# Kernel optimization log

Hardware: AMD Instinct MI355X
Metric: run time of the kernel (lower is better)

The kernel has to match this reference:

```python
import jax, jax.numpy as jnp
import numpy as np

HID = 512
ROLES = 64

def setup_inputs() -> dict:
    key = jax.random.key(0)
    k1, k2, k3, k4, k5 = jax.random.split(key, 5)
    pred_input = jax.random.normal(k1, (8, 512, HID), dtype=jnp.float32)
    args_input = jax.random.normal(k2, (8, 512, HID), dtype=jnp.float32)
    # learned params (orthogonal init approximated by scaled normal for testing)
    U = jax.random.normal(k3, (HID, ROLES, HID), dtype=jnp.float32) * 0.02
    bias1 = jax.random.normal(k4, (1, HID * ROLES), dtype=jnp.float32) * 0.02
    bias2 = jax.random.normal(k5, (1, ROLES), dtype=jnp.float32) * 0.02
    return {"pred_input": pred_input, "args_input": args_input,
            "U": U, "bias1": bias1, "bias2": bias2}

def reference(pred_input, args_input, U, bias1, bias2):
    # dropout p=0.0 -> identity (eval behavior)
    b, t, h = pred_input.shape
    n = b * t
    pred = pred_input.reshape(n, h)          # [n, h]
    args = args_input.reshape(n, h)          # [n, h]
    # first = pred @ U.view(h, R*h) + bias1  -> [n, R*h]
    first = pred @ U.reshape(h, -1) + bias1
    # batched bilinear reduction: [n, R, h] x [n, h] -> [n, R]
    out = jnp.einsum('nrk,nk->nr', first.reshape(n, ROLES, h), args)
    return out + bias2
```

## Files before the change

### kernel.cpp

```cpp
#include <hip/hip_runtime.h>
#include <stdint.h>


#define HID   512
#define ROLES 64
#define NTOK  4096
#define BM    256
#define BN    256
#define BK    64

typedef __attribute__((ext_vector_type(8))) _Float16 f16x8;
typedef __attribute__((ext_vector_type(4))) _Float16 f16x4;
typedef __attribute__((ext_vector_type(4))) float    f32x4;

__device__ __forceinline__ void async16(const void* g, void* l) {
  __builtin_amdgcn_global_load_lds(
      (const __attribute__((address_space(1))) uint32_t*)g,
      (__attribute__((address_space(3))) uint32_t*)l, 16, 0, 0);
}

__global__ __launch_bounds__(256) void prep_fused(
    const float* __restrict__ pred_in, _Float16* __restrict__ predf,
    const float* __restrict__ U, _Float16* __restrict__ ut) {
  __shared__ float tile[128][65];
  const int bx = blockIdx.x;
  const int t  = threadIdx.x;

  if (bx >= 2048) {
    const int idx = (bx - 2048) * 256 + t;
    const float4 v = ((const float4*)pred_in)[idx];
    f16x4 o;
    o[0] = (_Float16)v.x; o[1] = (_Float16)v.y;
    o[2] = (_Float16)v.z; o[3] = (_Float16)v.w;
    ((f16x4*)predf)[idx] = o;
    return;
  }

  const int kb = bx & 7, hb = (bx >> 3) & 3, r = bx >> 5;
  const int h0 = hb * 128, k0 = kb * 64;
  const int rr = t >> 4, c4 = (t & 15) * 4;
#pragma unroll
  for (int pass = 0; pass < 8; pass++) {
    const int row = pass * 16 + rr;
    const float4 v = *(const float4*)(U + ((size_t)(h0 + row) * ROLES + r) * HID + k0 + c4);
    tile[row][c4 + 0] = v.x; tile[row][c4 + 1] = v.y;
    tile[row][c4 + 2] = v.z; tile[row][c4 + 3] = v.w;
  }
  __syncthreads();
  const int kr = t >> 4, hc = (t & 15) * 8;
#pragma unroll
  for (int pass = 0; pass < 4; pass++) {
    const int k = pass * 16 + kr;
    alignas(16) _Float16 hbuf[8];
#pragma unroll
    for (int j = 0; j < 8; j++) hbuf[j] = (_Float16)tile[hc + j][k];
    *(uint4*)(ut + ((size_t)r * HID + k0 + k) * HID + h0 + hc) = *(const uint4*)hbuf;
  }
}

__global__ __launch_bounds__(512, 2) void bilinear_mfma(
    const _Float16* __restrict__ predf, const _Float16* __restrict__ utf,
    const float* __restrict__ args, const float* __restrict__ bias1,
    float* __restrict__ part) {
  __shared__ _Float16 lds[2][32768];

  const int nblk = blockIdx.x, mblk = blockIdx.y, r = blockIdx.z;
  const int m0 = mblk * BM, n0 = nblk * BN;
  const int tid  = threadIdx.x;
  const int lane = tid & 63, wid = tid >> 6;
  const int col  = lane & 15, quad = lane >> 4;
  const int wr = wid >> 2, wc = wid & 3;
  const int wm = wr * 128, wn = wc * 64;

  const int i_loc = tid >> 3;
  const int ko    = ((tid & 7) ^ (i_loc & 7)) * 8;
  const size_t offA = (size_t)(m0 + i_loc) * HID + ko;
  const size_t offB = ((size_t)r * HID + n0 + i_loc) * HID + ko;
  const int ldsOff = tid * 8;

  const int slotL8 = (quad ^ (col & 7)) * 8;
  const int slotH8 = slotL8 ^ 32;
  int rowA[8], rowB[4];
#pragma unroll
  for (int mt = 0; mt < 8; mt++) rowA[mt] = (wm + mt * 16 + col) * BK;
#pragma unroll
  for (int nt = 0; nt < 4; nt++) rowB[nt] = (wn + nt * 16 + col) * BK;

  f32x4 acc[8][4];
#pragma unroll
  for (int a = 0; a < 8; a++)
#pragma unroll
    for (int b = 0; b < 4; b++) acc[a][b] = (f32x4){0.f, 0.f, 0.f, 0.f};

  auto STAGE = [&](int t, int buf) {
    _Float16* bA = &lds[buf][0];
    _Float16* bB = &lds[buf][16384];
    const size_t kof = (size_t)t * BK;
#pragma unroll
    for (int c = 0; c < 4; c++) {
      async16(predf + offA + (size_t)(c * 64) * HID + kof, bA + c * 4096 + ldsOff);
      async16(utf   + offB + (size_t)(c * 64) * HID + kof, bB + c * 4096 + ldsOff);
    }
  };

  STAGE(0, 0);
  STAGE(1, 1);
  asm volatile("s_waitcnt vmcnt(8)" ::: "memory");
  __builtin_amdgcn_s_barrier();
  __builtin_amdgcn_sched_barrier(0);

  for (int t = 0; t < 8; ++t) {
    const _Float16* bA = &lds[t & 1][0];
    const _Float16* bB = &lds[t & 1][16384];

    f16x8 aL[4], aH[4], bL[2], bH[2], cL[2], cH[2];

#pragma unroll
    for (int mt = 0; mt < 4; mt++) {
      aL[mt] = *(const f16x8*)(bA + rowA[mt] + slotL8);
      aH[mt] = *(const f16x8*)(bA + rowA[mt] + slotH8);
    }
#pragma unroll
    for (int nt = 0; nt < 2; nt++) {
      bL[nt] = *(const f16x8*)(bB + rowB[nt] + slotL8);
      bH[nt] = *(const f16x8*)(bB + rowB[nt] + slotH8);
    }
    __builtin_amdgcn_s_setprio(1);
#pragma unroll
    for (int mt = 0; mt < 4; mt++)
#pragma unroll
      for (int nt = 0; nt < 2; nt++) {
        acc[mt][nt] = __builtin_amdgcn_mfma_f32_16x16x32_f16(aL[mt], bL[nt], acc[mt][nt], 0, 0, 0);
        acc[mt][nt] = __builtin_amdgcn_mfma_f32_16x16x32_f16(aH[mt], bH[nt], acc[mt][nt], 0, 0, 0);
      }
    __builtin_amdgcn_s_setprio(0);
    __builtin_amdgcn_s_barrier();
    __builtin_amdgcn_sched_barrier(0);

#pragma unroll
    for (int nt = 0; nt < 2; nt++) {
      cL[nt] = *(const f16x8*)(bB + rowB[nt + 2] + slotL8);
      cH[nt] = *(const f16x8*)(bB + rowB[nt + 2] + slotH8);
    }
    __builtin_amdgcn_s_setprio(1);
#pragma unroll
    for (int mt = 0; mt < 4; mt++)
#pragma unroll
      for (int nt = 0; nt < 2; nt++) {
        acc[mt][nt + 2] = __builtin_amdgcn_mfma_f32_16x16x32_f16(aL[mt], cL[nt], acc[mt][nt + 2], 0, 0, 0);
        acc[mt][nt + 2] = __builtin_amdgcn_mfma_f32_16x16x32_f16(aH[mt], cH[nt], acc[mt][nt + 2], 0, 0, 0);
      }
    __builtin_amdgcn_s_setprio(0);
    __builtin_amdgcn_s_barrier();
    __builtin_amdgcn_sched_barrier(0);

#pragma unroll
    for (int mt = 0; mt < 4; mt++) {
      aL[mt] = *(const f16x8*)(bA + rowA[mt + 4] + slotL8);
      aH[mt] = *(const f16x8*)(bA + rowA[mt + 4] + slotH8);
    }
    __builtin_amdgcn_s_setprio(1);
#pragma unroll
    for (int mt = 0; mt < 4; mt++)
#pragma unroll
      for (int nt = 0; nt < 2; nt++) {
        acc[mt + 4][nt + 2] = __builtin_amdgcn_mfma_f32_16x16x32_f16(aL[mt], cL[nt], acc[mt + 4][nt + 2], 0, 0, 0);
        acc[mt + 4][nt + 2] = __builtin_amdgcn_mfma_f32_16x16x32_f16(aH[mt], cH[nt], acc[mt + 4][nt + 2], 0, 0, 0);
      }
    __builtin_amdgcn_s_setprio(0);
    __builtin_amdgcn_s_barrier();
    __builtin_amdgcn_sched_barrier(0);

#pragma unroll
    for (int nt = 0; nt < 2; nt++) {
      bL[nt] = *(const f16x8*)(bB + rowB[nt] + slotL8);
      bH[nt] = *(const f16x8*)(bB + rowB[nt] + slotH8);
    }
    __builtin_amdgcn_s_setprio(1);
#pragma unroll
    for (int mt = 0; mt < 4; mt++)
#pragma unroll
      for (int nt = 0; nt < 2; nt++) {
        acc[mt + 4][nt] = __builtin_amdgcn_mfma_f32_16x16x32_f16(aL[mt], bL[nt], acc[mt + 4][nt], 0, 0, 0);
        acc[mt + 4][nt] = __builtin_amdgcn_mfma_f32_16x16x32_f16(aH[mt], bH[nt], acc[mt + 4][nt], 0, 0, 0);
      }
    __builtin_amdgcn_s_setprio(0);
    __builtin_amdgcn_s_barrier();
    __builtin_amdgcn_sched_barrier(0);

    if (t < 6) {
      STAGE(t + 2, t & 1);
      asm volatile("s_waitcnt vmcnt(8)" ::: "memory");
    } else if (t == 6) {
      asm volatile("s_waitcnt vmcnt(0)" ::: "memory");
    }
    __builtin_amdgcn_s_barrier();
    __builtin_amdgcn_sched_barrier(0);
  }

  float b1v[4];
#pragma unroll
  for (int nt = 0; nt < 4; nt++)
    b1v[nt] = bias1[r * HID + n0 + wn + nt * 16 + col];

  float sval[8][4];
#pragma unroll
  for (int mt = 0; mt < 8; mt++) {
#pragma unroll
    for (int reg = 0; reg < 4; reg++) {
      const int m = m0 + wm + mt * 16 + quad * 4 + reg;
      const float* arow = args + (size_t)m * HID + n0 + wn + col;
      float s = 0.f;
#pragma unroll
      for (int nt = 0; nt < 4; nt++)
        s += (acc[mt][nt][reg] + b1v[nt]) * arow[nt * 16];
      s += __shfl_xor(s, 1);
      s += __shfl_xor(s, 2);
      s += __shfl_xor(s, 4);
      s += __shfl_xor(s, 8);
      sval[mt][reg] = s;
    }
  }

  float* red = (float*)&lds[0][0];
  if (wc != 0 && col == 0) {
#pragma unroll
    for (int mt = 0; mt < 8; mt++)
#pragma unroll
      for (int reg = 0; reg < 4; reg++)
        red[(wc - 1) * 256 + wm + mt * 16 + quad * 4 + reg] = sval[mt][reg];
  }
  __syncthreads();
  if (wc == 0 && col == 0) {
    float* pbase = part + (((size_t)nblk * ROLES + r) << 12) + m0;
#pragma unroll
    for (int mt = 0; mt < 8; mt++) {
      const int row = wm + mt * 16 + quad * 4;
      float4 v;
      v.x = sval[mt][0] + red[row + 0] + red[256 + row + 0] + red[512 + row + 0];
      v.y = sval[mt][1] + red[row + 1] + red[256 + row + 1] + red[512 + row + 1];
      v.z = sval[mt][2] + red[row + 2] + red[256 + row + 2] + red[512 + row + 2];
      v.w = sval[mt][3] + red[row + 3] + red[256 + row + 3] + red[512 + row + 3];
      *(float4*)(pbase + row) = v;
    }
  }
}

__global__ __launch_bounds__(256) void reduce_k(const float* __restrict__ part,
                                                const float* __restrict__ b2,
                                                float* __restrict__ out) {
  const int idx = blockIdx.x * 256 + threadIdx.x;
  const int m = idx >> 6, r = idx & (ROLES - 1);
  float v = b2[r];
#pragma unroll
  for (int nb = 0; nb < 2; nb++)
    v += part[(((size_t)nb * ROLES + r) << 12) + m];
  out[idx] = v;
}

__global__ __launch_bounds__(256) void fallback_k(
    const float* __restrict__ pred, const float* __restrict__ args,
    const float* __restrict__ U, const float* __restrict__ b1,
    const float* __restrict__ b2, float* __restrict__ out) {
  const int idx = blockIdx.x * 256 + threadIdx.x;
  const int r = idx >> 12;
  const int n = idx & (NTOK - 1);
  const float* arow = args + (size_t)n * HID;
  const float* prow = pred + (size_t)n * HID;
  float acc = 0.f;
  for (int h = 0; h < HID; h++) {
    const float* urow = U + ((size_t)h * ROLES + r) * HID;
    float s = 0.f;
    for (int k = 0; k < HID; k++) s = fmaf(urow[k], arow[k], s);
    acc = fmaf(prow[h], s, acc);
  }
  float sb = 0.f;
  const float* brow = b1 + (size_t)r * HID;
  for (int k = 0; k < HID; k++) sb = fmaf(brow[k], arow[k], sb);
  out[(size_t)n * ROLES + r] = acc + sb + b2[r];
}

extern "C" void kernel_launch(void* const* d_in, const int* in_sizes, int n_in,
                              void* d_out, int out_size, void* d_ws, size_t ws_size,
                              hipStream_t stream) {
  const float* pred = (const float*)d_in[0];
  const float* args = (const float*)d_in[1];
  const float* U    = (const float*)d_in[2];
  const float* b1   = (const float*)d_in[3];
  const float* b2   = (const float*)d_in[4];
  float* out = (float*)d_out;

  const size_t PRED_ELEMS = (size_t)NTOK * HID;
  const size_t U_ELEMS    = (size_t)HID * ROLES * HID;
  const size_t PART_ELEMS = (size_t)2 * ROLES * NTOK;
  const size_t WS_NEEDED  = (PRED_ELEMS + U_ELEMS) * sizeof(_Float16)
                          + PART_ELEMS * sizeof(float);

  if (ws_size < WS_NEEDED) {
    hipLaunchKernelGGL(fallback_k, dim3((NTOK * ROLES) / 256), dim3(256), 0, stream,
                       pred, args, U, b1, b2, out);
    return;
  }

  _Float16* predf = (_Float16*)d_ws;
  _Float16* utf   = predf + PRED_ELEMS;
  float*    partb = (float*)(utf + U_ELEMS);

  hipLaunchKernelGGL(prep_fused, dim3(4096), dim3(256), 0, stream,
                     pred, predf, U, utf);
  hipLaunchKernelGGL(bilinear_mfma, dim3(HID / BN, NTOK / BM, ROLES), dim3(512), 0, stream,
                     predf, utf, args, b1, partb);
  hipLaunchKernelGGL(reduce_k, dim3((NTOK * ROLES) / 256), dim3(256), 0, stream,
                     partb, b2, out);
}
```

Before: 267.1 us.

## Loop both N halves inside each block and fold bias2 in, dropping reduce kernel

Each block now loops over both 256-wide N halves of the hidden dimension and keeps a running per-row bilinear sum. Bias2 is added in the epilogue, which writes the output directly, so the partial buffer and the separate reduce kernel go away. This saves one launch and a round trip to global memory. In exchange the grid is halved (1024 blocks), so parallelism and latency hiding drop, and the output writes are strided by ROLES and scattered rather than issued as float4 stores.

```diff
diff --git a/kernel.cpp b/kernel.cpp
--- a/kernel.cpp
+++ b/kernel.cpp
@@ -61,11 +61,11 @@
 __global__ __launch_bounds__(512, 2) void bilinear_mfma(
     const _Float16* __restrict__ predf, const _Float16* __restrict__ utf,
     const float* __restrict__ args, const float* __restrict__ bias1,
-    float* __restrict__ part) {
+    const float* __restrict__ bias2, float* __restrict__ out) {
   __shared__ _Float16 lds[2][32768];
 
-  const int nblk = blockIdx.x, mblk = blockIdx.y, r = blockIdx.z;
-  const int m0 = mblk * BM, n0 = nblk * BN;
+  const int mblk = blockIdx.x, r = blockIdx.y;
+  const int m0 = mblk * BM;
   const int tid  = threadIdx.x;
   const int lane = tid & 63, wid = tid >> 6;
   const int col  = lane & 15, quad = lane >> 4;
@@ -74,8 +74,8 @@
 
   const int i_loc = tid >> 3;
   const int ko    = ((tid & 7) ^ (i_loc & 7)) * 8;
-  const size_t offA = (size_t)(m0 + i_loc) * HID + ko;
-  const size_t offB = ((size_t)r * HID + n0 + i_loc) * HID + ko;
+  const size_t offA  = (size_t)(m0 + i_loc) * HID + ko;
+  const size_t offB0 = ((size_t)r * HID + i_loc) * HID + ko;
   const int ldsOff = tid * 8;
 
   const int slotL8 = (quad ^ (col & 7)) * 8;
@@ -86,139 +86,149 @@
 #pragma unroll
   for (int nt = 0; nt < 4; nt++) rowB[nt] = (wn + nt * 16 + col) * BK;
 
-  f32x4 acc[8][4];
+  float sval[8][4];
 #pragma unroll
   for (int a = 0; a < 8; a++)
 #pragma unroll
-    for (int b = 0; b < 4; b++) acc[a][b] = (f32x4){0.f, 0.f, 0.f, 0.f};
-
-  auto STAGE = [&](int t, int buf) {
-    _Float16* bA = &lds[buf][0];
-    _Float16* bB = &lds[buf][16384];
-    const size_t kof = (size_t)t * BK;
-#pragma unroll
-    for (int c = 0; c < 4; c++) {
-      async16(predf + offA + (size_t)(c * 64) * HID + kof, bA + c * 4096 + ldsOff);
-      async16(utf   + offB + (size_t)(c * 64) * HID + kof, bB + c * 4096 + ldsOff);
-    }
-  };
-
-  STAGE(0, 0);
-  STAGE(1, 1);
-  asm volatile("s_waitcnt vmcnt(8)" ::: "memory");
-  __builtin_amdgcn_s_barrier();
-  __builtin_amdgcn_sched_barrier(0);
-
-  for (int t = 0; t < 8; ++t) {
-    const _Float16* bA = &lds[t & 1][0];
-    const _Float16* bB = &lds[t & 1][16384];
-
-    f16x8 aL[4], aH[4], bL[2], bH[2], cL[2], cH[2];
-
-#pragma unroll
-    for (int mt = 0; mt < 4; mt++) {
-      aL[mt] = *(const f16x8*)(bA + rowA[mt] + slotL8);
-      aH[mt] = *(const f16x8*)(bA + rowA[mt] + slotH8);
-    }
-#pragma unroll
-    for (int nt = 0; nt < 2; nt++) {
-      bL[nt] = *(const f16x8*)(bB + rowB[nt] + slotL8);
-      bH[nt] = *(const f16x8*)(bB + rowB[nt] + slotH8);
-    }
-    __builtin_amdgcn_s_setprio(1);
-#pragma unroll
-    for (int mt = 0; mt < 4; mt++)
-#pragma unroll
-      for (int nt = 0; nt < 2; nt++) {
-        acc[mt][nt] = __builtin_amdgcn_mfma_f32_16x16x32_f16(aL[mt], bL[nt], acc[mt][nt], 0, 0, 0);
-        acc[mt][nt] = __builtin_amdgcn_mfma_f32_16x16x32_f16(aH[mt], bH[nt], acc[mt][nt], 0, 0, 0);
-      }
-    __builtin_amdgcn_s_setprio(0);
+    for (int b = 0; b < 4; b++) sval[a][b] = 0.f;
+
+  for (int half = 0; half < 2; ++half) {
+    const int n0 = half * BN;
+    const size_t offB = offB0 + (size_t)n0 * HID;
+
+    f32x4 acc[8][4];
+#pragma unroll
+    for (int a = 0; a < 8; a++)
+#pragma unroll
+      for (int b = 0; b < 4; b++) acc[a][b] = (f32x4){0.f, 0.f, 0.f, 0.f};
+
+    auto STAGE = [&](int t, int buf) {
+      _Float16* bA = &lds[buf][0];
+      _Float16* bB = &lds[buf][16384];
+      const size_t kof = (size_t)t * BK;
+#pragma unroll
+      for (int c = 0; c < 4; c++) {
+        async16(predf + offA + (size_t)(c * 64) * HID + kof, bA + c * 4096 + ldsOff);
+        async16(utf   + offB + (size_t)(c * 64) * HID + kof, bB + c * 4096 + ldsOff);
+      }
+    };
+
+    STAGE(0, 0);
+    STAGE(1, 1);
+    asm volatile("s_waitcnt vmcnt(8)" ::: "memory");
     __builtin_amdgcn_s_barrier();
     __builtin_amdgcn_sched_barrier(0);
 
-#pragma unroll
-    for (int nt = 0; nt < 2; nt++) {
-      cL[nt] = *(const f16x8*)(bB + rowB[nt + 2] + slotL8);
-      cH[nt] = *(const f16x8*)(bB + rowB[nt + 2] + slotH8);
+    for (int t = 0; t < 8; ++t) {
+      const _Float16* bA = &lds[t & 1][0];
+      const _Float16* bB = &lds[t & 1][16384];
+
+      f16x8 aL[4], aH[4], bL[2], bH[2], cL[2], cH[2];
+
+#pragma unroll
+      for (int mt = 0; mt < 4; mt++) {
+        aL[mt] = *(const f16x8*)(bA + rowA[mt] + slotL8);
+        aH[mt] = *(const f16x8*)(bA + rowA[mt] + slotH8);
+      }
+#pragma unroll
+      for (int nt = 0; nt < 2; nt++) {
+        bL[nt] = *(const f16x8*)(bB + rowB[nt] + slotL8);
+        bH[nt] = *(const f16x8*)(bB + rowB[nt] + slotH8);
+      }
+      __builtin_amdgcn_s_setprio(1);
+#pragma unroll
+      for (int mt = 0; mt < 4; mt++)
+#pragma unroll
+        for (int nt = 0; nt < 2; nt++) {
+          acc[mt][nt] = __builtin_amdgcn_mfma_f32_16x16x32_f16(aL[mt], bL[nt], acc[mt][nt], 0, 0, 0);
+          acc[mt][nt] = __builtin_amdgcn_mfma_f32_16x16x32_f16(aH[mt], bH[nt], acc[mt][nt], 0, 0, 0);
+        }
+      __builtin_amdgcn_s_setprio(0);
+      __builtin_amdgcn_s_barrier();
+      __builtin_amdgcn_sched_barrier(0);
+
+#pragma unroll
+      for (int nt = 0; nt < 2; nt++) {
+        cL[nt] = *(const f16x8*)(bB + rowB[nt + 2] + slotL8);
+        cH[nt] = *(const f16x8*)(bB + rowB[nt + 2] + slotH8);
+      }
+      __builtin_amdgcn_s_setprio(1);
+#pragma unroll
+      for (int mt = 0; mt < 4; mt++)
+#pragma unroll
+        for (int nt = 0; nt < 2; nt++) {
+          acc[mt][nt + 2] = __builtin_amdgcn_mfma_f32_16x16x32_f16(aL[mt], cL[nt], acc[mt][nt + 2], 0, 0, 0);
+          acc[mt][nt + 2] = __builtin_amdgcn_mfma_f32_16x16x32_f16(aH[mt], cH[nt], acc[mt][nt + 2], 0, 0, 0);
+        }
+      __builtin_amdgcn_s_setprio(0);
+      __builtin_amdgcn_s_barrier();
+      __builtin_amdgcn_sched_barrier(0);
+
+#pragma unroll
+      for (int mt = 0; mt < 4; mt++) {
+        aL[mt] = *(const f16x8*)(bA + rowA[mt + 4] + slotL8);
+        aH[mt] = *(const f16x8*)(bA + rowA[mt + 4] + slotH8);
+      }
+      __builtin_amdgcn_s_setprio(1);
+#pragma unroll
+      for (int mt = 0; mt < 4; mt++)
+#pragma unroll
+        for (int nt = 0; nt < 2; nt++) {
+          acc[mt + 4][nt + 2] = __builtin_amdgcn_mfma_f32_16x16x32_f16(aL[mt], cL[nt], acc[mt + 4][nt + 2], 0, 0, 0);
+          acc[mt + 4][nt + 2] = __builtin_amdgcn_mfma_f32_16x16x32_f16(aH[mt], cH[nt], acc[mt + 4][nt + 2], 0, 0, 0);
+        }
+      __builtin_amdgcn_s_setprio(0);
+      __builtin_amdgcn_s_barrier();
+      __builtin_amdgcn_sched_barrier(0);
+
+#pragma unroll
+      for (int nt = 0; nt < 2; nt++) {
+        bL[nt] = *(const f16x8*)(bB + rowB[nt] + slotL8);
+        bH[nt] = *(const f16x8*)(bB + rowB[nt] + slotH8);
+      }
+      __builtin_amdgcn_s_setprio(1);
+#pragma unroll
+      for (int mt = 0; mt < 4; mt++)
+#pragma unroll
+        for (int nt = 0; nt < 2; nt++) {
+          acc[mt + 4][nt] = __builtin_amdgcn_mfma_f32_16x16x32_f16(aL[mt], bL[nt], acc[mt + 4][nt], 0, 0, 0);
+          acc[mt + 4][nt] = __builtin_amdgcn_mfma_f32_16x16x32_f16(aH[mt], bH[nt], acc[mt + 4][nt], 0, 0, 0);
+        }
+      __builtin_amdgcn_s_setprio(0);
+      __builtin_amdgcn_s_barrier();
+      __builtin_amdgcn_sched_barrier(0);
+
+      if (t < 6) {
+        STAGE(t + 2, t & 1);
+        asm volatile("s_waitcnt vmcnt(8)" ::: "memory");
+      } else if (t == 6) {
+        asm volatile("s_waitcnt vmcnt(0)" ::: "memory");
+      }
+      __builtin_amdgcn_s_barrier();
+      __builtin_amdgcn_sched_barrier(0);
     }
-    __builtin_amdgcn_s_setprio(1);
-#pragma unroll
-    for (int mt = 0; mt < 4; mt++)
-#pragma unroll
-      for (int nt = 0; nt < 2; nt++) {
-        acc[mt][nt + 2] = __builtin_amdgcn_mfma_f32_16x16x32_f16(aL[mt], cL[nt], acc[mt][nt + 2], 0, 0, 0);
-        acc[mt][nt + 2] = __builtin_amdgcn_mfma_f32_16x16x32_f16(aH[mt], cH[nt], acc[mt][nt + 2], 0, 0, 0);
-      }
-    __builtin_amdgcn_s_setprio(0);
-    __builtin_amdgcn_s_barrier();
-    __builtin_amdgcn_sched_barrier(0);
-
-#pragma unroll
-    for (int mt = 0; mt < 4; mt++) {
-      aL[mt] = *(const f16x8*)(bA + rowA[mt + 4] + slotL8);
-      aH[mt] = *(const f16x8*)(bA + rowA[mt + 4] + slotH8);
-    }
-    __builtin_amdgcn_s_setprio(1);
-#pragma unroll
-    for (int mt = 0; mt < 4; mt++)
-#pragma unroll
-      for (int nt = 0; nt < 2; nt++) {
-        acc[mt + 4][nt + 2] = __builtin_amdgcn_mfma_f32_16x16x32_f16(aL[mt], cL[nt], acc[mt + 4][nt + 2], 0, 0, 0);
-        acc[mt + 4][nt + 2] = __builtin_amdgcn_mfma_f32_16x16x32_f16(aH[mt], cH[nt], acc[mt + 4][nt + 2], 0, 0, 0);
-      }
-    __builtin_amdgcn_s_setprio(0);
-    __builtin_amdgcn_s_barrier();
-    __builtin_amdgcn_sched_barrier(0);
-
-#pragma unroll
-    for (int nt = 0; nt < 2; nt++) {
-      bL[nt] = *(const f16x8*)(bB + rowB[nt] + slotL8);
-      bH[nt] = *(const f16x8*)(bB + rowB[nt] + slotH8);
-    }
-    __builtin_amdgcn_s_setprio(1);
-#pragma unroll
-    for (int mt = 0; mt < 4; mt++)
-#pragma unroll
-      for (int nt = 0; nt < 2; nt++) {
-        acc[mt + 4][nt] = __builtin_amdgcn_mfma_f32_16x16x32_f16(aL[mt], bL[nt], acc[mt + 4][nt], 0, 0, 0);
-        acc[mt + 4][nt] = __builtin_amdgcn_mfma_f32_16x16x32_f16(aH[mt], bH[nt], acc[mt + 4][nt], 0, 0, 0);
-      }
-    __builtin_amdgcn_s_setprio(0);
-    __builtin_amdgcn_s_barrier();
-    __builtin_amdgcn_sched_barrier(0);
-
-    if (t < 6) {
-      STAGE(t + 2, t & 1);
-      asm volatile("s_waitcnt vmcnt(8)" ::: "memory");
-    } else if (t == 6) {
-      asm volatile("s_waitcnt vmcnt(0)" ::: "memory");
-    }
-    __builtin_amdgcn_s_barrier();
-    __builtin_amdgcn_sched_barrier(0);
-  }
-
-  float b1v[4];
-#pragma unroll
-  for (int nt = 0; nt < 4; nt++)
-    b1v[nt] = bias1[r * HID + n0 + wn + nt * 16 + col];
-
-  float sval[8][4];
-#pragma unroll
-  for (int mt = 0; mt < 8; mt++) {
-#pragma unroll
-    for (int reg = 0; reg < 4; reg++) {
-      const int m = m0 + wm + mt * 16 + quad * 4 + reg;
-      const float* arow = args + (size_t)m * HID + n0 + wn + col;
-      float s = 0.f;
-#pragma unroll
-      for (int nt = 0; nt < 4; nt++)
-        s += (acc[mt][nt][reg] + b1v[nt]) * arow[nt * 16];
-      s += __shfl_xor(s, 1);
-      s += __shfl_xor(s, 2);
-      s += __shfl_xor(s, 4);
-      s += __shfl_xor(s, 8);
-      sval[mt][reg] = s;
+
+    float b1v[4];
+#pragma unroll
+    for (int nt = 0; nt < 4; nt++)
+      b1v[nt] = bias1[r * HID + n0 + wn + nt * 16 + col];
+
+#pragma unroll
+    for (int mt = 0; mt < 8; mt++) {
+#pragma unroll
+      for (int reg = 0; reg < 4; reg++) {
+        const int m = m0 + wm + mt * 16 + quad * 4 + reg;
+        const float* arow = args + (size_t)m * HID + n0 + wn + col;
+        float s = 0.f;
+#pragma unroll
+        for (int nt = 0; nt < 4; nt++)
+          s += (acc[mt][nt][reg] + b1v[nt]) * arow[nt * 16];
+        s += __shfl_xor(s, 1);
+        s += __shfl_xor(s, 2);
+        s += __shfl_xor(s, 4);
+        s += __shfl_xor(s, 8);
+        sval[mt][reg] += s;
+      }
     }
   }
 
@@ -232,30 +242,17 @@
   }
   __syncthreads();
   if (wc == 0 && col == 0) {
-    float* pbase = part + (((size_t)nblk * ROLES + r) << 12) + m0;
+    const float b2v = bias2[r];
 #pragma unroll
     for (int mt = 0; mt < 8; mt++) {
-      const int row = wm + mt * 16 + quad * 4;
-      float4 v;
-      v.x = sval[mt][0] + red[row + 0] + red[256 + row + 0] + red[512 + row + 0];
-      v.y = sval[mt][1] + red[row + 1] + red[256 + row + 1] + red[512 + row + 1];
-      v.z = sval[mt][2] + red[row + 2] + red[256 + row + 2] + red[512 + row + 2];
-      v.w = sval[mt][3] + red[row + 3] + red[256 + row + 3] + red[512 + row + 3];
-      *(float4*)(pbase + row) = v;
+#pragma unroll
+      for (int reg = 0; reg < 4; reg++) {
+        const int row = wm + mt * 16 + quad * 4 + reg;
+        out[(size_t)(m0 + row) * ROLES + r] =
+            sval[mt][reg] + red[row] + red[256 + row] + red[512 + row] + b2v;
+      }
     }
   }
-}
-
-__global__ __launch_bounds__(256) void reduce_k(const float* __restrict__ part,
-                                                const float* __restrict__ b2,
-                                                float* __restrict__ out) {
-  const int idx = blockIdx.x * 256 + threadIdx.x;
-  const int m = idx >> 6, r = idx & (ROLES - 1);
-  float v = b2[r];
-#pragma unroll
-  for (int nb = 0; nb < 2; nb++)
-    v += part[(((size_t)nb * ROLES + r) << 12) + m];
-  out[idx] = v;
 }
 
 __global__ __launch_bounds__(256) void fallback_k(
@@ -292,9 +289,7 @@
 
   const size_t PRED_ELEMS = (size_t)NTOK * HID;
   const size_t U_ELEMS    = (size_t)HID * ROLES * HID;
-  const size_t PART_ELEMS = (size_t)2 * ROLES * NTOK;
-  const size_t WS_NEEDED  = (PRED_ELEMS + U_ELEMS) * sizeof(_Float16)
-                          + PART_ELEMS * sizeof(float);
+  const size_t WS_NEEDED  = (PRED_ELEMS + U_ELEMS) * sizeof(_Float16);
 
   if (ws_size < WS_NEEDED) {
     hipLaunchKernelGGL(fallback_k, dim3((NTOK * ROLES) / 256), dim3(256), 0, stream,
@@ -304,12 +299,9 @@
 
   _Float16* predf = (_Float16*)d_ws;
   _Float16* utf   = predf + PRED_ELEMS;
-  float*    partb = (float*)(utf + U_ELEMS);
 
   hipLaunchKernelGGL(prep_fused, dim3(4096), dim3(256), 0, stream,
                      pred, predf, U, utf);
-  hipLaunchKernelGGL(bilinear_mfma, dim3(HID / BN, NTOK / BM, ROLES), dim3(512), 0, stream,
-                     predf, utf, args, b1, partb);
-  hipLaunchKernelGGL(reduce_k, dim3((NTOK * ROLES) / 256), dim3(256), 0, stream,
-                     partb, b2, out);
-}
+  hipLaunchKernelGGL(bilinear_mfma, dim3(NTOK / BM, ROLES), dim3(512), 0, stream,
+                     predf, utf, args, b1, b2, out);
+}
```

After: 450.4 us. 68.7% more time.
